# Kernel tuning notes

Hardware: AMD Instinct MI355X
Metric: run time of the kernel (lower is better)

The kernel has to match this reference:

```python
import jax, jax.numpy as jnp
import numpy as np

B, T, E, H = 2, 2048, 1024, 16
D = E // H  # head_size

def setup_inputs() -> dict:
    key = jax.random.key(0)
    ks = jax.random.split(key, 6)
    s = 0.02
    return {
        "x":  jax.random.normal(ks[0], (B, T, E), dtype=jnp.float32),
        "Wq": jax.random.normal(ks[1], (E, E), dtype=jnp.float32) * s,
        "Wk": jax.random.normal(ks[2], (E, E), dtype=jnp.float32) * s,
        "Wv": jax.random.normal(ks[3], (E, E), dtype=jnp.float32) * s,
        "Wp": jax.random.normal(ks[4], (E, E), dtype=jnp.float32) * s,
        "bp": jnp.zeros((E,), dtype=jnp.float32),
    }

def reference(x, Wq, Wk, Wv, Wp, bp):
    b, t, e = x.shape
    # Per-head Linear(E, D, bias=False) stacked == single [E,E] matmul then head split.
    # torch Linear: y = x @ W.T
    q = (x @ Wq.T).reshape(b, t, H, D).transpose(0, 2, 1, 3)  # (B,H,T,D)
    k = (x @ Wk.T).reshape(b, t, H, D).transpose(0, 2, 1, 3)
    v = (x @ Wv.T).reshape(b, t, H, D).transpose(0, 2, 1, 3)
    scale = jnp.asarray(D, x.dtype) ** -0.5
    wei = jnp.einsum('bhqd,bhkd->bhqk', q, k) * scale  # (B,H,T,T)
    causal = jnp.tril(jnp.ones((t, t), dtype=bool))
    wei = jnp.where(causal, wei, -jnp.inf)
    wei = jax.nn.softmax(wei, axis=-1)
    # dropout p=0.0 -> identity (eval-mode determinism)
    out = jnp.einsum('bhqk,bhkd->bhqd', wei, v)  # (B,H,T,D)
    out = out.transpose(0, 2, 1, 3).reshape(b, t, e)  # concat heads
    return out @ Wp.T + bp
```

## Files before the change

### kernel.cpp

```cpp
#include <hip/hip_runtime.h>

#define T_ 2048
#define E_ 1024
#define H_ 16
#define D_ 64
#define M_ 4096

typedef unsigned short ushort_t;
typedef __attribute__((ext_vector_type(8))) short bf16x8;
typedef __attribute__((ext_vector_type(4))) float f32x4;
typedef __attribute__((ext_vector_type(4))) unsigned short u16x4;
typedef __attribute__((ext_vector_type(8))) unsigned short u16x8;
typedef __attribute__((ext_vector_type(2))) unsigned int u32x2;

__device__ __forceinline__ ushort_t f2bf(float f) {
  union { float f; unsigned u; } v; v.f = f;
  unsigned r = v.u + 0x7FFFu + ((v.u >> 16) & 1u);
  return (ushort_t)(r >> 16);
}

__device__ __forceinline__ void gl16(const void* g, void* l) {
  __builtin_amdgcn_global_load_lds((const __attribute__((address_space(1))) void*)g,
                                   (__attribute__((address_space(3))) void*)l, 16, 0, 0);
}

__global__ __launch_bounds__(256)
void conv_all(const float* __restrict__ x,  const float* __restrict__ wq,
              const float* __restrict__ wk, const float* __restrict__ wv,
              const float* __restrict__ wp,
              ushort_t* __restrict__ xb,  ushort_t* __restrict__ wqb,
              ushort_t* __restrict__ wkb, ushort_t* __restrict__ wvb,
              ushort_t* __restrict__ wpb)
{
  const int id = blockIdx.x;
  const float* s; ushort_t* d; size_t off;
  if (id < 2048) { s = x; d = xb; off = (size_t)id * 2048; }
  else {
    int wsel = (id - 2048) >> 9, wid = (id - 2048) & 511;
    off = (size_t)wid * 2048;
    s = wsel == 0 ? wq : wsel == 1 ? wk : wsel == 2 ? wv : wp;
    d = wsel == 0 ? wqb : wsel == 1 ? wkb : wsel == 2 ? wvb : wpb;
  }
  size_t i = off + (size_t)threadIdx.x * 8;
  float4 a = *(const float4*)(s + i);
  float4 b = *(const float4*)(s + i + 4);
  u16x8 o;
  o[0]=f2bf(a.x); o[1]=f2bf(a.y); o[2]=f2bf(a.z); o[3]=f2bf(a.w);
  o[4]=f2bf(b.x); o[5]=f2bf(b.y); o[6]=f2bf(b.z); o[7]=f2bf(b.w);
  *(u16x8*)(d + i) = o;
}

__device__ __forceinline__ void gemm_core(const ushort_t* __restrict__ A,
                                          const ushort_t* __restrict__ W,
                                          int m0, int n0,
                                          ushort_t* As, ushort_t* Bs,
                                          f32x4 acc[4][4])
{
  const int t = threadIdx.x;
  const int lane = t & 63, w = t >> 6;
  const int g = lane >> 4, lq = lane & 15;
  const int wr = w >> 1, wc = w & 1;
  const int r0 = t >> 2;
  const int c0 = t & 3;
  const int ca0 = c0 ^ ((r0 >> 1) & 3);
  const int r1 = r0 + 64;
  const int ca1 = c0 ^ ((r1 >> 1) & 3);

  #pragma unroll
  for (int i = 0; i < 4; ++i)
    #pragma unroll
    for (int j = 0; j < 4; ++j) acc[i][j] = (f32x4){0.f,0.f,0.f,0.f};

  for (int k0 = 0; k0 < 1024; k0 += 32) {
    __syncthreads();
    gl16(A + (size_t)(m0 + r0) * 1024 + k0 + ca0 * 8, As + t * 8);
    gl16(A + (size_t)(m0 + r1) * 1024 + k0 + ca1 * 8, As + 2048 + t * 8);
    gl16(W + (size_t)(n0 + r0) * 1024 + k0 + ca0 * 8, Bs + t * 8);
    gl16(W + (size_t)(n0 + r1) * 1024 + k0 + ca1 * 8, Bs + 2048 + t * 8);
    __syncthreads();

    bf16x8 af[4], bfr[4];
    #pragma unroll
    for (int mi = 0; mi < 4; ++mi) {
      int row = wr * 64 + mi * 16 + lq;
      int ch = g ^ ((row >> 1) & 3);
      af[mi] = *(const bf16x8*)(As + row * 32 + ch * 8);
    }
    #pragma unroll
    for (int ni = 0; ni < 4; ++ni) {
      int row = wc * 64 + ni * 16 + lq;
      int ch = g ^ ((row >> 1) & 3);
      bfr[ni] = *(const bf16x8*)(Bs + row * 32 + ch * 8);
    }
    __builtin_amdgcn_s_setprio(1);
    #pragma unroll
    for (int mi = 0; mi < 4; ++mi)
      #pragma unroll
      for (int ni = 0; ni < 4; ++ni)
        acc[mi][ni] = __builtin_amdgcn_mfma_f32_16x16x32_bf16(af[mi], bfr[ni], acc[mi][ni], 0, 0, 0);
    __builtin_amdgcn_s_setprio(0);
  }
}

__global__ __launch_bounds__(256)
void gemm_qkv(const ushort_t* __restrict__ xb,
              const ushort_t* __restrict__ wqb, const ushort_t* __restrict__ wkb,
              const ushort_t* __restrict__ wvb,
              ushort_t* __restrict__ Qd, ushort_t* __restrict__ Kd, ushort_t* __restrict__ Vd)
{
  __shared__ __align__(16) ushort_t As[4096];
  __shared__ __align__(16) ushort_t Bs[4096];
  const int bx = blockIdx.x;
  const int sel = bx >> 3;
  const int n0 = (bx & 7) * 128;
  const int m0 = blockIdx.y * 128;
  const ushort_t* W = sel == 0 ? wqb : (sel == 1 ? wkb : wvb);
  f32x4 acc[4][4];
  gemm_core(xb, W, m0, n0, As, Bs, acc);

  const int t = threadIdx.x, lane = t & 63, w = t >> 6;
  const int g = lane >> 4, lq = lane & 15, wr = w >> 1, wc = w & 1;
  const float scl = (sel == 0) ? 0.125f : 1.0f;
  ushort_t* dst = sel == 0 ? Qd : (sel == 1 ? Kd : Vd);
  #pragma unroll
  for (int mi = 0; mi < 4; ++mi)
    #pragma unroll
    for (int ni = 0; ni < 4; ++ni)
      #pragma unroll
      for (int r = 0; r < 4; ++r) {
        int m = m0 + wr * 64 + mi * 16 + 4 * g + r;
        int n = n0 + wc * 64 + ni * 16 + lq;
        int b = m >> 11, tt = m & (T_ - 1);
        int h = n >> 6, d = n & (D_ - 1);
        ushort_t v = f2bf(acc[mi][ni][r] * scl);
        if (sel < 2) dst[((size_t)(b * H_ + h) * T_ + tt) * D_ + d] = v;
        else         dst[((size_t)(b * H_ + h) * D_ + d) * T_ + tt] = v;
      }
}

__global__ __launch_bounds__(256)
void gemm_out64(const ushort_t* __restrict__ Ab, const ushort_t* __restrict__ wpb,
                const float* __restrict__ bias, float* __restrict__ out)
{
  __shared__ __align__(16) ushort_t As[2048];
  __shared__ __align__(16) ushort_t Bs[4096];
  const int t = threadIdx.x, lane = t & 63, w = t >> 6;
  const int g = lane >> 4, lq = lane & 15;
  const int n0 = blockIdx.x * 128;
  const int m0 = blockIdx.y * 64;
  const int r0 = t >> 2, c0 = t & 3;
  const int ca0 = c0 ^ ((r0 >> 1) & 3);
  const int r1 = r0 + 64;
  const int ca1 = c0 ^ ((r1 >> 1) & 3);

  f32x4 acc[4][2];
  #pragma unroll
  for (int i = 0; i < 4; ++i) { acc[i][0] = (f32x4){0.f,0.f,0.f,0.f}; acc[i][1] = (f32x4){0.f,0.f,0.f,0.f}; }

  for (int k0 = 0; k0 < 1024; k0 += 32) {
    __syncthreads();
    gl16(Ab  + (size_t)(m0 + r0) * 1024 + k0 + ca0 * 8, As + t * 8);
    gl16(wpb + (size_t)(n0 + r0) * 1024 + k0 + ca0 * 8, Bs + t * 8);
    gl16(wpb + (size_t)(n0 + r1) * 1024 + k0 + ca1 * 8, Bs + 2048 + t * 8);
    __syncthreads();

    bf16x8 af[4], bfr[2];
    #pragma unroll
    for (int mi = 0; mi < 4; ++mi) {
      int row = mi * 16 + lq;
      int ch = g ^ ((row >> 1) & 3);
      af[mi] = *(const bf16x8*)(As + row * 32 + ch * 8);
    }
    #pragma unroll
    for (int ni = 0; ni < 2; ++ni) {
      int row = w * 32 + ni * 16 + lq;
      int ch = g ^ ((row >> 1) & 3);
      bfr[ni] = *(const bf16x8*)(Bs + row * 32 + ch * 8);
    }
    __builtin_amdgcn_s_setprio(1);
    #pragma unroll
    for (int mi = 0; mi < 4; ++mi)
      #pragma unroll
      for (int ni = 0; ni < 2; ++ni)
        acc[mi][ni] = __builtin_amdgcn_mfma_f32_16x16x32_bf16(af[mi], bfr[ni], acc[mi][ni], 0, 0, 0);
    __builtin_amdgcn_s_setprio(0);
  }
  #pragma unroll
  for (int mi = 0; mi < 4; ++mi)
    #pragma unroll
    for (int ni = 0; ni < 2; ++ni)
      #pragma unroll
      for (int r = 0; r < 4; ++r) {
        int m = m0 + mi * 16 + 4 * g + r;
        int n = n0 + w * 32 + ni * 16 + lq;
        out[(size_t)m * E_ + n] = acc[mi][ni][r] + bias[n];
      }
}

__global__ __launch_bounds__(256)
void attn_mfma(const ushort_t* __restrict__ Q, const ushort_t* __restrict__ K,
               const ushort_t* __restrict__ Vt, ushort_t* __restrict__ O)
{
  __shared__ __align__(16) ushort_t Ks[2][4096];
  __shared__ __align__(16) ushort_t Vs[2][4096];
  __shared__ __align__(16) ushort_t Ps[128 * 72];
  const int t = threadIdx.x, w = t >> 6, lane = t & 63;
  const int g = lane >> 4, lq = lane & 15;
  const int bh = blockIdx.y;
  const int qt = 15 - ((blockIdx.x + bh) & 15);
  const int q0 = qt * 128;
  const size_t qkbase = (size_t)bh * T_ * D_;
  const size_t vbase  = (size_t)bh * D_ * T_;

  const int srow = t >> 3, sc = t & 7;
  const int cs0 = sc ^ (srow & 7);
  const int srow1 = srow + 32;
  const int cs1 = sc ^ (srow1 & 7);

  const int rowA = 32 * w + lq, rowB = rowA + 16;
  const int qgA = q0 + rowA, qgB = q0 + rowB;
  const bf16x8 qA0 = *(const bf16x8*)(Q + qkbase + (size_t)qgA * D_ + g * 8);
  const bf16x8 qA1 = *(const bf16x8*)(Q + qkbase + (size_t)qgA * D_ + 32 + g * 8);
  const bf16x8 qB0 = *(const bf16x8*)(Q + qkbase + (size_t)qgB * D_ + g * 8);
  const bf16x8 qB1 = *(const bf16x8*)(Q + qkbase + (size_t)qgB * D_ + 32 + g * 8);

  f32x4 accA[4], accB[4];
  #pragma unroll
  for (int db = 0; db < 4; ++db) { accA[db] = (f32x4){0.f,0.f,0.f,0.f}; accB[db] = (f32x4){0.f,0.f,0.f,0.f}; }
  float mA = -1e30f, lA = 0.f, mB = -1e30f, lB = 0.f;

  const int nt = 2 * qt + 2;

  {
    gl16(K + qkbase + (size_t)srow  * D_ + cs0 * 8, &Ks[0][t * 8]);
    gl16(K + qkbase + (size_t)srow1 * D_ + cs1 * 8, &Ks[0][2048 + t * 8]);
    gl16(Vt + vbase + (size_t)srow  * T_ + cs0 * 8, &Vs[0][t * 8]);
    gl16(Vt + vbase + (size_t)srow1 * T_ + cs1 * 8, &Vs[0][2048 + t * 8]);
  }
  __syncthreads();

  for (int kt = 0; kt < nt; ++kt) {
    const int cur = kt & 1;
    const int k0 = kt * 64;
    if (kt + 1 < nt) {
      const int kn = (kt + 1) * 64;
      gl16(K + qkbase + (size_t)(kn + srow)  * D_ + cs0 * 8, &Ks[cur ^ 1][t * 8]);
      gl16(K + qkbase + (size_t)(kn + srow1) * D_ + cs1 * 8, &Ks[cur ^ 1][2048 + t * 8]);
      gl16(Vt + vbase + (size_t)srow  * T_ + kn + cs0 * 8, &Vs[cur ^ 1][t * 8]);
      gl16(Vt + vbase + (size_t)srow1 * T_ + kn + cs1 * 8, &Vs[cur ^ 1][2048 + t * 8]);
    }
    const ushort_t* kb_ = &Ks[cur][0];
    const ushort_t* vb_ = &Vs[cur][0];

    f32x4 stA[4], stB[4];
    __builtin_amdgcn_s_setprio(1);
    #pragma unroll
    for (int kb = 0; kb < 4; ++kb) {
      int krow = kb * 16 + lq;
      bf16x8 ka0 = *(const bf16x8*)(kb_ + krow * 64 + ((g ^ (krow & 7)) * 8));
      bf16x8 ka1 = *(const bf16x8*)(kb_ + krow * 64 + (((4 + g) ^ (krow & 7)) * 8));
      f32x4 zA = (f32x4){0.f,0.f,0.f,0.f};
      zA = __builtin_amdgcn_mfma_f32_16x16x32_bf16(ka0, qA0, zA, 0, 0, 0);
      zA = __builtin_amdgcn_mfma_f32_16x16x32_bf16(ka1, qA1, zA, 0, 0, 0);
      stA[kb] = zA;
      f32x4 zB = (f32x4){0.f,0.f,0.f,0.f};
      zB = __builtin_amdgcn_mfma_f32_16x16x32_bf16(ka0, qB0, zB, 0, 0, 0);
      zB = __builtin_amdgcn_mfma_f32_16x16x32_bf16(ka1, qB1, zB, 0, 0, 0);
      stB[kb] = zB;
    }
    __builtin_amdgcn_s_setprio(0);

    if (kt >= nt - 2) {
      #pragma unroll
      for (int kb = 0; kb < 4; ++kb)
        #pragma unroll
        for (int r = 0; r < 4; ++r) {
          int kg = k0 + kb * 16 + 4 * g + r;
          if (kg > qgA) stA[kb][r] = -1e30f;
          if (kg > qgB) stB[kb][r] = -1e30f;
        }
    }

    float tmA = -1e30f, tmB = -1e30f;
    #pragma unroll
    for (int kb = 0; kb < 4; ++kb)
      #pragma unroll
      for (int r = 0; r < 4; ++r) { tmA = fmaxf(tmA, stA[kb][r]); tmB = fmaxf(tmB, stB[kb][r]); }
    tmA = fmaxf(tmA, __shfl_xor(tmA, 16)); tmA = fmaxf(tmA, __shfl_xor(tmA, 32));
    tmB = fmaxf(tmB, __shfl_xor(tmB, 16)); tmB = fmaxf(tmB, __shfl_xor(tmB, 32));

    if (!__all((tmA <= mA + 8.f) && (tmB <= mB + 8.f))) {
      float mnA = fmaxf(mA, tmA), mnB = fmaxf(mB, tmB);
      float alA = __expf(mA - mnA), alB = __expf(mB - mnB);
      mA = mnA; mB = mnB;
      lA *= alA; lB *= alB;
      float alAr[4], alBr[4];
      #pragma unroll
      for (int r = 0; r < 4; ++r) { alAr[r] = __shfl(alA, 4 * g + r); alBr[r] = __shfl(alB, 4 * g + r); }
      #pragma unroll
      for (int db = 0; db < 4; ++db)
        #pragma unroll
        for (int r = 0; r < 4; ++r) { accA[db][r] *= alAr[r]; accB[db][r] *= alBr[r]; }
    }

    float tsA = 0.f, tsB = 0.f;
    #pragma unroll
    for (int kb = 0; kb < 4; ++kb) {
      float pA0 = __expf(stA[kb][0] - mA), pA1 = __expf(stA[kb][1] - mA);
      float pA2 = __expf(stA[kb][2] - mA), pA3 = __expf(stA[kb][3] - mA);
      float pB0 = __expf(stB[kb][0] - mB), pB1 = __expf(stB[kb][1] - mB);
      float pB2 = __expf(stB[kb][2] - mB), pB3 = __expf(stB[kb][3] - mB);
      tsA += (pA0 + pA1) + (pA2 + pA3);
      tsB += (pB0 + pB1) + (pB2 + pB3);
      unsigned aLo, aHi, bLo, bHi;
      asm("v_cvt_pk_bf16_f32 %0, %1, %2" : "=v"(aLo) : "v"(pA0), "v"(pA1));
      asm("v_cvt_pk_bf16_f32 %0, %1, %2" : "=v"(aHi) : "v"(pA2), "v"(pA3));
      asm("v_cvt_pk_bf16_f32 %0, %1, %2" : "=v"(bLo) : "v"(pB0), "v"(pB1));
      asm("v_cvt_pk_bf16_f32 %0, %1, %2" : "=v"(bHi) : "v"(pB2), "v"(pB3));
      *(u32x2*)(Ps + rowA * 72 + kb * 16 + 4 * g) = (u32x2){aLo, aHi};
      *(u32x2*)(Ps + rowB * 72 + kb * 16 + 4 * g) = (u32x2){bLo, bHi};
    }
    tsA += __shfl_xor(tsA, 16); tsA += __shfl_xor(tsA, 32);
    tsB += __shfl_xor(tsB, 16); tsB += __shfl_xor(tsB, 32);
    lA += tsA; lB += tsB;

    asm volatile("s_waitcnt lgkmcnt(0)" ::: "memory");
    bf16x8 paA0 = *(const bf16x8*)(Ps + rowA * 72 + g * 8);
    bf16x8 paA1 = *(const bf16x8*)(Ps + rowA * 72 + 32 + g * 8);
    bf16x8 paB0 = *(const bf16x8*)(Ps + rowB * 72 + g * 8);
    bf16x8 paB1 = *(const bf16x8*)(Ps + rowB * 72 + 32 + g * 8);

    __builtin_amdgcn_s_setprio(1);
    #pragma unroll
    for (int db = 0; db < 4; ++db) {
      int vrow = db * 16 + lq;
      bf16x8 vb0 = *(const bf16x8*)(vb_ + vrow * 64 + ((g ^ (vrow & 7)) * 8));
      bf16x8 vb1 = *(const bf16x8*)(vb_ + vrow * 64 + (((4 + g) ^ (vrow & 7)) * 8));
      accA[db] = __builtin_amdgcn_mfma_f32_16x16x32_bf16(paA0, vb0, accA[db], 0, 0, 0);
      accA[db] = __builtin_amdgcn_mfma_f32_16x16x32_bf16(paA1, vb1, accA[db], 0, 0, 0);
      accB[db] = __builtin_amdgcn_mfma_f32_16x16x32_bf16(paB0, vb0, accB[db], 0, 0, 0);
      accB[db] = __builtin_amdgcn_mfma_f32_16x16x32_bf16(paB1, vb1, accB[db], 0, 0, 0);
    }
    __builtin_amdgcn_s_setprio(0);

    __syncthreads();
  }

  float invA = 1.0f / lA, invB = 1.0f / lB;
  float liA[4], liB[4];
  #pragma unroll
  for (int r = 0; r < 4; ++r) { liA[r] = __shfl(invA, 4 * g + r); liB[r] = __shfl(invB, 4 * g + r); }
  const int b = bh >> 4, h = bh & 15;
  #pragma unroll
  for (int db = 0; db < 4; ++db)
    #pragma unroll
    for (int r = 0; r < 4; ++r) {
      int mAo = q0 + 32 * w + 4 * g + r;
      int mBo = mAo + 16;
      O[((size_t)(b * T_ + mAo)) * E_ + h * 64 + db * 16 + lq] = f2bf(accA[db][r] * liA[r]);
      O[((size_t)(b * T_ + mBo)) * E_ + h * 64 + db * 16 + lq] = f2bf(accB[db][r] * liB[r]);
    }
}

extern "C" void kernel_launch(void* const* d_in, const int* in_sizes, int n_in,
                              void* d_out, int out_size, void* d_ws, size_t ws_size,
                              hipStream_t stream) {
  const float* x  = (const float*)d_in[0];
  const float* Wq = (const float*)d_in[1];
  const float* Wk = (const float*)d_in[2];
  const float* Wv = (const float*)d_in[3];
  const float* Wp = (const float*)d_in[4];
  const float* bp = (const float*)d_in[5];
  float* out = (float*)d_out;

  ushort_t* ws  = (ushort_t*)d_ws;
  ushort_t* xb  = ws;
  ushort_t* wqb = xb  + (size_t)M_ * E_;
  ushort_t* wkb = wqb + (size_t)E_ * E_;
  ushort_t* wvb = wkb + (size_t)E_ * E_;
  ushort_t* wpb = wvb + (size_t)E_ * E_;
  ushort_t* Qb  = wpb + (size_t)E_ * E_;
  ushort_t* Kb  = Qb  + (size_t)M_ * E_;
  ushort_t* Vb  = Kb  + (size_t)M_ * E_;
  ushort_t* Ab  = Vb  + (size_t)M_ * E_;

  conv_all<<<4096, 256, 0, stream>>>(x, Wq, Wk, Wv, Wp, xb, wqb, wkb, wvb, wpb);
  gemm_qkv<<<dim3(24, 32), 256, 0, stream>>>(xb, wqb, wkb, wvb, Qb, Kb, Vb);
  attn_mfma<<<dim3(16, 32), 256, 0, stream>>>(Qb, Kb, Vb, Ab);
  gemm_out64<<<dim3(8, 64), 256, 0, stream>>>(Ab, wpb, bp, out);
}
```

Measured before the change: 138.4 us.

## Load K/V fragments directly to registers and remap attention grid per XCD

The attention kernel drops its double-buffered LDS staging of K and V. Each wave now loads its K and V MFMA fragments straight from global memory into registers, and the per-iteration block barrier is removed, since the P scratch rows are private to each wave. The grid becomes 1D with an XCD-aware mapping: each XCD handles four heads, and q-tiles run in a mixed ascending/descending order to balance the causal work. Launch bounds now request two blocks per CU. The aim is to remove barrier and LDS overhead and improve L2 locality, at the cost of four-fold redundant global/L2 reads across waves and no explicit prefetch, so load latency is exposed.

```diff
diff --git a/kernel.cpp b/kernel.cpp
--- a/kernel.cpp
+++ b/kernel.cpp
@@ -197,25 +197,20 @@
       }
 }
 
-__global__ __launch_bounds__(256)
+__global__ __launch_bounds__(256, 2)
 void attn_mfma(const ushort_t* __restrict__ Q, const ushort_t* __restrict__ K,
                const ushort_t* __restrict__ Vt, ushort_t* __restrict__ O)
 {
-  __shared__ __align__(16) ushort_t Ks[2][4096];
-  __shared__ __align__(16) ushort_t Vs[2][4096];
   __shared__ __align__(16) ushort_t Ps[128 * 72];
   const int t = threadIdx.x, w = t >> 6, lane = t & 63;
   const int g = lane >> 4, lq = lane & 15;
-  const int bh = blockIdx.y;
-  const int qt = 15 - ((blockIdx.x + bh) & 15);
+  const int i = blockIdx.x;
+  const int xcd = i & 7, chunk = i >> 3;
+  const int bh = xcd * 4 + (chunk >> 4);
+  const int qt = (chunk < 32) ? (chunk & 15) : (15 - (chunk & 15));
   const int q0 = qt * 128;
   const size_t qkbase = (size_t)bh * T_ * D_;
   const size_t vbase  = (size_t)bh * D_ * T_;
-
-  const int srow = t >> 3, sc = t & 7;
-  const int cs0 = sc ^ (srow & 7);
-  const int srow1 = srow + 32;
-  const int cs1 = sc ^ (srow1 & 7);
 
   const int rowA = 32 * w + lq, rowB = rowA + 16;
   const int qgA = q0 + rowA, qgB = q0 + rowB;
@@ -231,41 +226,34 @@
 
   const int nt = 2 * qt + 2;
 
-  {
-    gl16(K + qkbase + (size_t)srow  * D_ + cs0 * 8, &Ks[0][t * 8]);
-    gl16(K + qkbase + (size_t)srow1 * D_ + cs1 * 8, &Ks[0][2048 + t * 8]);
-    gl16(Vt + vbase + (size_t)srow  * T_ + cs0 * 8, &Vs[0][t * 8]);
-    gl16(Vt + vbase + (size_t)srow1 * T_ + cs1 * 8, &Vs[0][2048 + t * 8]);
-  }
-  __syncthreads();
-
   for (int kt = 0; kt < nt; ++kt) {
-    const int cur = kt & 1;
     const int k0 = kt * 64;
-    if (kt + 1 < nt) {
-      const int kn = (kt + 1) * 64;
-      gl16(K + qkbase + (size_t)(kn + srow)  * D_ + cs0 * 8, &Ks[cur ^ 1][t * 8]);
-      gl16(K + qkbase + (size_t)(kn + srow1) * D_ + cs1 * 8, &Ks[cur ^ 1][2048 + t * 8]);
-      gl16(Vt + vbase + (size_t)srow  * T_ + kn + cs0 * 8, &Vs[cur ^ 1][t * 8]);
-      gl16(Vt + vbase + (size_t)srow1 * T_ + kn + cs1 * 8, &Vs[cur ^ 1][2048 + t * 8]);
-    }
-    const ushort_t* kb_ = &Ks[cur][0];
-    const ushort_t* vb_ = &Vs[cur][0];
+
+    bf16x8 kf0[4], kf1[4], vf0[4], vf1[4];
+    #pragma unroll
+    for (int kb = 0; kb < 4; ++kb) {
+      const ushort_t* kp = K + qkbase + (size_t)(k0 + kb * 16 + lq) * D_;
+      kf0[kb] = *(const bf16x8*)(kp + g * 8);
+      kf1[kb] = *(const bf16x8*)(kp + 32 + g * 8);
+    }
+    #pragma unroll
+    for (int db = 0; db < 4; ++db) {
+      const ushort_t* vp = Vt + vbase + (size_t)(db * 16 + lq) * T_ + k0;
+      vf0[db] = *(const bf16x8*)(vp + g * 8);
+      vf1[db] = *(const bf16x8*)(vp + 32 + g * 8);
+    }
 
     f32x4 stA[4], stB[4];
     __builtin_amdgcn_s_setprio(1);
     #pragma unroll
     for (int kb = 0; kb < 4; ++kb) {
-      int krow = kb * 16 + lq;
-      bf16x8 ka0 = *(const bf16x8*)(kb_ + krow * 64 + ((g ^ (krow & 7)) * 8));
-      bf16x8 ka1 = *(const bf16x8*)(kb_ + krow * 64 + (((4 + g) ^ (krow & 7)) * 8));
       f32x4 zA = (f32x4){0.f,0.f,0.f,0.f};
-      zA = __builtin_amdgcn_mfma_f32_16x16x32_bf16(ka0, qA0, zA, 0, 0, 0);
-      zA = __builtin_amdgcn_mfma_f32_16x16x32_bf16(ka1, qA1, zA, 0, 0, 0);
+      zA = __builtin_amdgcn_mfma_f32_16x16x32_bf16(kf0[kb], qA0, zA, 0, 0, 0);
+      zA = __builtin_amdgcn_mfma_f32_16x16x32_bf16(kf1[kb], qA1, zA, 0, 0, 0);
       stA[kb] = zA;
       f32x4 zB = (f32x4){0.f,0.f,0.f,0.f};
-      zB = __builtin_amdgcn_mfma_f32_16x16x32_bf16(ka0, qB0, zB, 0, 0, 0);
-      zB = __builtin_amdgcn_mfma_f32_16x16x32_bf16(ka1, qB1, zB, 0, 0, 0);
+      zB = __builtin_amdgcn_mfma_f32_16x16x32_bf16(kf0[kb], qB0, zB, 0, 0, 0);
+      zB = __builtin_amdgcn_mfma_f32_16x16x32_bf16(kf1[kb], qB1, zB, 0, 0, 0);
       stB[kb] = zB;
     }
     __builtin_amdgcn_s_setprio(0);
@@ -333,17 +321,12 @@
     __builtin_amdgcn_s_setprio(1);
     #pragma unroll
     for (int db = 0; db < 4; ++db) {
-      int vrow = db * 16 + lq;
-      bf16x8 vb0 = *(const bf16x8*)(vb_ + vrow * 64 + ((g ^ (vrow & 7)) * 8));
-      bf16x8 vb1 = *(const bf16x8*)(vb_ + vrow * 64 + (((4 + g) ^ (vrow & 7)) * 8));
-      accA[db] = __builtin_amdgcn_mfma_f32_16x16x32_bf16(paA0, vb0, accA[db], 0, 0, 0);
-      accA[db] = __builtin_amdgcn_mfma_f32_16x16x32_bf16(paA1, vb1, accA[db], 0, 0, 0);
-      accB[db] = __builtin_amdgcn_mfma_f32_16x16x32_bf16(paB0, vb0, accB[db], 0, 0, 0);
-      accB[db] = __builtin_amdgcn_mfma_f32_16x16x32_bf16(paB1, vb1, accB[db], 0, 0, 0);
+      accA[db] = __builtin_amdgcn_mfma_f32_16x16x32_bf16(paA0, vf0[db], accA[db], 0, 0, 0);
+      accA[db] = __builtin_amdgcn_mfma_f32_16x16x32_bf16(paA1, vf1[db], accA[db], 0, 0, 0);
+      accB[db] = __builtin_amdgcn_mfma_f32_16x16x32_bf16(paB0, vf0[db], accB[db], 0, 0, 0);
+      accB[db] = __builtin_amdgcn_mfma_f32_16x16x32_bf16(paB1, vf1[db], accB[db], 0, 0, 0);
     }
     __builtin_amdgcn_s_setprio(0);
-
-    __syncthreads();
   }
 
   float invA = 1.0f / lA, invB = 1.0f / lB;
@@ -386,6 +369,6 @@
 
   conv_all<<<4096, 256, 0, stream>>>(x, Wq, Wk, Wv, Wp, xb, wqb, wkb, wvb, wpb);
   gemm_qkv<<<dim3(24, 32), 256, 0, stream>>>(xb, wqb, wkb, wvb, Qb, Kb, Vb);
-  attn_mfma<<<dim3(16, 32), 256, 0, stream>>>(Qb, Kb, Vb, Ab);
+  attn_mfma<<<512, 256, 0, stream>>>(Qb, Kb, Vb, Ab);
   gemm_out64<<<dim3(8, 64), 256, 0, stream>>>(Ab, wpb, bp, out);
 }
```

Result: no change. 137.1 us (-0.9%).
